# Optimization experiments

Measured on AMD Instinct MI355X. Metric: run time of the kernel, lower is better.

The kernel has to match this reference:

```python
import jax, jax.numpy as jnp
import numpy as np

N_NODES = 50000
N_EDGES = 800000
IN_CH = 128
HID = 32
HEADS = 4
OUT_CH = 10
N_GRAPHS = 64
NEG_SLOPE = 0.2  # PyG GATConv default


def setup_inputs() -> dict:
    key = jax.random.key(0)
    ks = jax.random.split(key, 16)
    d = {}
    d["x"] = jax.random.normal(ks[0], (N_NODES, IN_CH), dtype=jnp.float32)
    d["edge_index"] = jax.random.randint(ks[1], (2, N_EDGES), 0, N_NODES, dtype=jnp.int64)
    d["batch"] = jnp.sort(jax.random.randint(ks[2], (N_NODES,), 0, N_GRAPHS, dtype=jnp.int64))
    s1 = 1.0 / np.sqrt(IN_CH)
    s2 = 1.0 / np.sqrt(HEADS * HID)
    d["W1"] = jax.random.normal(ks[3], (IN_CH, HEADS * HID), dtype=jnp.float32) * s1
    d["att_src1"] = jax.random.normal(ks[4], (HEADS, HID), dtype=jnp.float32) * s2
    d["att_dst1"] = jax.random.normal(ks[5], (HEADS, HID), dtype=jnp.float32) * s2
    d["b1"] = jnp.zeros((HEADS * HID,), dtype=jnp.float32)
    d["W2"] = jax.random.normal(ks[6], (HEADS * HID, HEADS * HID), dtype=jnp.float32) * s2
    d["att_src2"] = jax.random.normal(ks[7], (HEADS, HID), dtype=jnp.float32) * s2
    d["att_dst2"] = jax.random.normal(ks[8], (HEADS, HID), dtype=jnp.float32) * s2
    d["b2"] = jnp.zeros((HEADS * HID,), dtype=jnp.float32)
    d["w_lin"] = jax.random.normal(ks[9], (HEADS * HID, OUT_CH), dtype=jnp.float32) * s2
    d["b_lin"] = jnp.zeros((OUT_CH,), dtype=jnp.float32)
    return d


def _gat_conv(x, src, dst, W, att_src, att_dst, bias):
    # x: [N, Fin] -> h: [N, H, C]
    h = (x @ W).reshape(N_NODES, HEADS, HID)
    a_src = jnp.sum(h * att_src, axis=-1)  # [N, H]
    a_dst = jnp.sum(h * att_dst, axis=-1)  # [N, H]
    e = jax.nn.leaky_relu(a_src[src] + a_dst[dst], NEG_SLOPE)  # [E, H]
    # segment softmax over incoming edges of each destination node
    e_max = jax.ops.segment_max(e, dst, num_segments=N_NODES)  # [N, H]
    e_exp = jnp.exp(e - e_max[dst])
    denom = jax.ops.segment_sum(e_exp, dst, num_segments=N_NODES)  # [N, H]
    alpha = e_exp / denom[dst]  # [E, H]
    # weighted scatter-add aggregation
    out = jax.ops.segment_sum(alpha[:, :, None] * h[src], dst, num_segments=N_NODES)
    return out.reshape(N_NODES, HEADS * HID) + bias


def reference(x, edge_index, batch, W1, att_src1, att_dst1, b1,
              W2, att_src2, att_dst2, b2, w_lin, b_lin):
    # PyG GATConv adds self loops by default
    loops = jnp.arange(N_NODES, dtype=edge_index.dtype)
    src = jnp.concatenate([edge_index[0], loops])
    dst = jnp.concatenate([edge_index[1], loops])

    h = jax.nn.relu(_gat_conv(x, src, dst, W1, att_src1, att_dst1, b1))
    h = jax.nn.relu(_gat_conv(h, src, dst, W2, att_src2, att_dst2, b2))

    # global mean pool over graphs
    sums = jax.ops.segment_sum(h, batch, num_segments=N_GRAPHS)  # [G, H*C]
    counts = jax.ops.segment_sum(jnp.ones((N_NODES,), dtype=h.dtype), batch,
                                 num_segments=N_GRAPHS)
    pooled = sums / jnp.maximum(counts, 1.0)[:, None]

    # dropout is identity in eval mode
    return pooled @ w_lin + b_lin
```

## Files before the change

### kernel.cpp

```cpp
#include <hip/hip_runtime.h>
#include <hip/hip_bf16.h>
#include <math.h>

constexpr int NN = 50000;
constexpr int NE = 800000;
constexpr int ET = NE + NN;
constexpr int FH = 128;
constexpr int NHEAD = 4;
constexpr int NG = 64;
constexpr int OC = 10;

constexpr int NBK = (NN + 255) >> 8;
constexpr int EPB = 4000;
constexpr int HBLK = NE / EPB;

constexpr int WKP = 136;
constexpr int WPLANE = 128 * WKP;

constexpr int GEMM1_GRID = (NN + 255) / 256;
constexpr int GEMM2_GRID = (NN + 63) / 64;

typedef __attribute__((ext_vector_type(8))) short short8;
typedef __attribute__((ext_vector_type(4))) float f32x4;

__device__ inline ushort f2bf_bits(float f) {
    union { __hip_bfloat16 h; ushort u; } c;
    c.h = __float2bfloat16(f);
    return c.u;
}

#define GEMM_EPILOGUE()                                                          \
    float as_[8], ad_[8];                                                        \
    _Pragma("unroll")                                                            \
    for (int t = 0; t < 8; ++t) {                                                \
        as_[t] = att_s[t * 16 + l16];                                            \
        ad_[t] = att_d[t * 16 + l16];                                            \
    }                                                                            \
    float hs[4][4], hd[4][4];                                                    \
    _Pragma("unroll")                                                            \
    for (int r = 0; r < 4; ++r) {                                                \
        int grow = row0 + quad * 4 + r;                                          \
        bool okr = (grow < NN);                                                  \
        _Pragma("unroll")                                                        \
        for (int h = 0; h < 4; ++h) {                                            \
            hs[r][h] = acc[2*h][r] * as_[2*h] + acc[2*h+1][r] * as_[2*h+1];      \
            hd[r][h] = acc[2*h][r] * ad_[2*h] + acc[2*h+1][r] * ad_[2*h+1];      \
        }                                                                        \
        if (okr) {                                                               \
            _Pragma("unroll")                                                    \
            for (int t = 0; t < 8; ++t)                                          \
                Hb[(size_t)grow * FH + t * 16 + l16] = __float2bfloat16(acc[t][r]); \
        }                                                                        \
    }                                                                            \
    _Pragma("unroll")                                                            \
    for (int o = 1; o < 16; o <<= 1) {                                           \
        _Pragma("unroll")                                                        \
        for (int r = 0; r < 4; ++r)                                              \
            _Pragma("unroll")                                                    \
            for (int h = 0; h < 4; ++h) {                                        \
                hs[r][h] += __shfl_xor(hs[r][h], o);                             \
                hd[r][h] += __shfl_xor(hd[r][h], o);                             \
            }                                                                    \
    }                                                                            \
    if (l16 == 0) {                                                              \
        _Pragma("unroll")                                                        \
        for (int r = 0; r < 4; ++r) {                                            \
            int grow = row0 + quad * 4 + r;                                      \
            if (grow < NN) {                                                     \
                *(float4*)&a_src[grow * NHEAD] = make_float4(hs[r][0], hs[r][1], hs[r][2], hs[r][3]); \
                *(float4*)&a_dst[grow * NHEAD] = make_float4(hd[r][0], hd[r][1], hd[r][2], hd[r][3]); \
            }                                                                    \
        }                                                                        \
    }

__global__ __launch_bounds__(1024) void fused_gemm_hist_kernel(
    const int* __restrict__ ei, int* __restrict__ blockHist,
    const float* __restrict__ A, const float* __restrict__ W1,
    const float* __restrict__ W2, ushort* __restrict__ wt,
    const float* __restrict__ att_s, const float* __restrict__ att_d,
    __hip_bfloat16* __restrict__ Hb, float* __restrict__ a_src, float* __restrict__ a_dst)
{
    __shared__ ushort Wlds[2 * WPLANE];
    const int tid = threadIdx.x;

    if (blockIdx.x >= GEMM1_GRID) {
        const int blk = blockIdx.x - GEMM1_GRID;
        int* hist = (int*)Wlds;
        if (tid < NBK) hist[tid] = 0;
        __syncthreads();
        const int e0 = blk * EPB;
        if (tid < EPB / 4) {
            int4 d4 = *(const int4*)(ei + NE + e0 + 4 * tid);
            atomicAdd(&hist[d4.x >> 8], 1);
            atomicAdd(&hist[d4.y >> 8], 1);
            atomicAdd(&hist[d4.z >> 8], 1);
            atomicAdd(&hist[d4.w >> 8], 1);
        }
        if (blk < 64 && tid < 256) {
            int idx = blk * 256 + tid;
            int k = idx >> 7, n = idx & 127;
            float f = W2[idx];
            ushort hb = f2bf_bits(f);
            union { ushort u; __hip_bfloat16 h; } c; c.u = hb;
            float lo = f - __bfloat162float(c.h);
            wt[n * WKP + k] = hb;
            wt[WPLANE + n * WKP + k] = f2bf_bits(lo);
        }
        __syncthreads();
        if (tid < NBK) blockHist[tid * HBLK + blk] = hist[tid];
        return;
    }

    for (int i = tid; i < FH * 128; i += 1024) {
        int k = i >> 7, n = i & 127;
        float f = W1[i];
        ushort hb = f2bf_bits(f);
        union { ushort u; __hip_bfloat16 h; } c; c.u = hb;
        float lo = f - __bfloat162float(c.h);
        Wlds[n * WKP + k] = hb;
        Wlds[WPLANE + n * WKP + k] = f2bf_bits(lo);
    }
    __syncthreads();

    const int wave = tid >> 6;
    const int lane = tid & 63;
    const int quad = lane >> 4;
    const int l16 = lane & 15;
    const int row0 = blockIdx.x * 256 + wave * 16;

    f32x4 acc[8];
#pragma unroll
    for (int t = 0; t < 8; ++t) acc[t] = (f32x4){0.f, 0.f, 0.f, 0.f};

    int arow = row0 + l16; if (arow >= NN) arow = NN - 1;
    const float* ap = A + (size_t)arow * FH + quad * 8;

#pragma unroll
    for (int kc = 0; kc < 4; ++kc) {
        float4 x0 = *(const float4*)(ap + kc * 32);
        float4 x1 = *(const float4*)(ap + kc * 32 + 4);
        float av[8] = {x0.x, x0.y, x0.z, x0.w, x1.x, x1.y, x1.z, x1.w};
        short8 ah, al;
#pragma unroll
        for (int j = 0; j < 8; ++j) {
            ushort hb = f2bf_bits(av[j]);
            union { ushort u; __hip_bfloat16 h; } c; c.u = hb;
            float lo = av[j] - __bfloat162float(c.h);
            ah[j] = (short)hb;
            al[j] = (short)f2bf_bits(lo);
        }
        const int kof = kc * 32 + quad * 8;
#pragma unroll
        for (int t = 0; t < 8; ++t) {
            const ushort* wp = &Wlds[(t * 16 + l16) * WKP + kof];
            short8 wh = *(const short8*)wp;
            short8 wl = *(const short8*)(wp + WPLANE);
            acc[t] = __builtin_amdgcn_mfma_f32_16x16x32_bf16(ah, wh, acc[t], 0, 0, 0);
            acc[t] = __builtin_amdgcn_mfma_f32_16x16x32_bf16(al, wh, acc[t], 0, 0, 0);
            acc[t] = __builtin_amdgcn_mfma_f32_16x16x32_bf16(ah, wl, acc[t], 0, 0, 0);
        }
    }
    GEMM_EPILOGUE()
}

__global__ __launch_bounds__(256) void scanAB_kernel(const int* __restrict__ bh,
                                                     int* __restrict__ bstart,
                                                     int* __restrict__ ebase,
                                                     int* __restrict__ offs) {
    __shared__ int sd[256];
    __shared__ int bprefix;
    const int b = blockIdx.x, t = threadIdx.x;
    int v = 0;
    if (t < NBK) {
        const int* p = bh + t * HBLK;
        for (int i = 0; i < HBLK; ++i) v += p[i];
    }
    sd[t] = v; __syncthreads();
#pragma unroll
    for (int o = 1; o < 256; o <<= 1) {
        int u = (t >= o) ? sd[t - o] : 0;
        __syncthreads();
        sd[t] += u;
        __syncthreads();
    }
    if (t == b) bprefix = sd[t] - v;
    if (b == 0) {
        if (t < NBK) ebase[t] = sd[t] - v;
        if (t == NBK - 1) ebase[NBK] = sd[t];
        if (t == 0) offs[NN] = ET;
    }
    __syncthreads();
    const int base = bprefix;
    __syncthreads();
    int c = (t < HBLK) ? bh[b * HBLK + t] : 0;
    sd[t] = c; __syncthreads();
#pragma unroll
    for (int o = 1; o < 256; o <<= 1) {
        int u = (t >= o) ? sd[t - o] : 0;
        __syncthreads();
        sd[t] += u;
        __syncthreads();
    }
    if (t < HBLK) bstart[b * HBLK + t] = base + sd[t] - c;
}

__global__ __launch_bounds__(1024) void bucket_scatter_kernel(
    const int* __restrict__ ei, const int* __restrict__ bstart,
    int2* __restrict__ ebuf) {
    __shared__ int cur[NBK];
    const int tid = threadIdx.x;
    const int blk = blockIdx.x;
    for (int i = tid; i < NBK; i += 1024) cur[i] = bstart[i * HBLK + blk];
    __syncthreads();
    const int e0 = blk * EPB;
    if (tid < EPB / 4) {
        int4 d4 = *(const int4*)(ei + NE + e0 + 4 * tid);
        int4 s4 = *(const int4*)(ei + e0 + 4 * tid);
        int ds[4] = {d4.x, d4.y, d4.z, d4.w};
        int ss[4] = {s4.x, s4.y, s4.z, s4.w};
#pragma unroll
        for (int j = 0; j < 4; ++j) {
            int pos = atomicAdd(&cur[ds[j] >> 8], 1);
            ebuf[pos] = make_int2(ss[j], ds[j]);
        }
    }
}

__global__ __launch_bounds__(256) void bucket_csr_kernel(
    const int2* __restrict__ ebuf, const int* __restrict__ ebase,
    int* __restrict__ offs, int* __restrict__ csrc) {
    __shared__ int hist[256];
    __shared__ int sd[256];
    __shared__ int cur[256];
    const int b = blockIdx.x, t = threadIdx.x;
    const int lo = b << 8;
    int psz = NN - lo; if (psz > 256) psz = 256;
    const int e0 = ebase[b], e1 = ebase[b + 1];

    hist[t] = 0;
    __syncthreads();
    for (int k = e0 + t; k < e1; k += 256) {
        int2 e = ebuf[k];
        atomicAdd(&hist[e.y - lo], 1);
    }
    __syncthreads();
    const int d = hist[t];
    sd[t] = d; __syncthreads();
#pragma unroll
    for (int o = 1; o < 256; o <<= 1) {
        int u = (t >= o) ? sd[t - o] : 0;
        __syncthreads();
        sd[t] += u;
        __syncthreads();
    }
    const int ex = sd[t] - d;
    if (t < psz) {
        const int node = lo + t;
        const int o = e0 + ex + node;
        offs[node] = o;
        cur[t] = o;
        csrc[o + d] = node;
    }
    __syncthreads();
    for (int k = e0 + t; k < e1; k += 256) {
        int2 e = ebuf[k];
        int pos = atomicAdd(&cur[e.y - lo], 1);
        csrc[pos] = e.x;
    }
}

__global__ __launch_bounds__(256) void gemm_att_bf16_kernel(
    const __hip_bfloat16* __restrict__ A, const ushort* __restrict__ wt,
    const float* __restrict__ att_s, const float* __restrict__ att_d,
    __hip_bfloat16* __restrict__ Hb, float* __restrict__ a_src, float* __restrict__ a_dst)
{
    __shared__ ushort Wlds[2 * WPLANE];
    const int tid = threadIdx.x;
    {
        const uint4* s = (const uint4*)wt;
        uint4* d = (uint4*)Wlds;
        for (int i = tid; i < 2 * WPLANE / 8; i += 256) d[i] = s[i];
    }
    __syncthreads();

    const int wave = tid >> 6;
    const int lane = tid & 63;
    const int quad = lane >> 4;
    const int l16 = lane & 15;
    const int row0 = blockIdx.x * 64 + wave * 16;

    f32x4 acc[8];
#pragma unroll
    for (int t = 0; t < 8; ++t) acc[t] = (f32x4){0.f, 0.f, 0.f, 0.f};

    int arow = row0 + l16; if (arow >= NN) arow = NN - 1;
    const __hip_bfloat16* ap = A + (size_t)arow * FH + quad * 8;

#pragma unroll
    for (int kc = 0; kc < 4; ++kc) {
        short8 ah = *(const short8*)(ap + kc * 32);
        const int kof = kc * 32 + quad * 8;
#pragma unroll
        for (int t = 0; t < 8; ++t) {
            const ushort* wp = &Wlds[(t * 16 + l16) * WKP + kof];
            short8 wh = *(const short8*)wp;
            short8 wl = *(const short8*)(wp + WPLANE);
            acc[t] = __builtin_amdgcn_mfma_f32_16x16x32_bf16(ah, wh, acc[t], 0, 0, 0);
            acc[t] = __builtin_amdgcn_mfma_f32_16x16x32_bf16(ah, wl, acc[t], 0, 0, 0);
        }
    }
    GEMM_EPILOGUE()
}

__global__ __launch_bounds__(256) void gat_agg_kernel(
    const __hip_bfloat16* __restrict__ Hb, const float* __restrict__ asrc,
    const float* __restrict__ adst, const int* __restrict__ offs,
    const int* __restrict__ csrc, const float* __restrict__ bias,
    __hip_bfloat16* __restrict__ out)
{
    const int wid = threadIdx.x >> 6;
    const int lane = threadIdx.x & 63;
    const int n = blockIdx.x * 4 + wid;

    const int beg = offs[n], end = offs[n + 1];
    const int es = lane >> 4;
    const int fs = lane & 15;
    const int hC = fs >> 2;
    const int f8 = fs * 8;
    const float adC = adst[n * NHEAD + hC];

    float dsum = 0.f;
    float acc[8];
#pragma unroll
    for (int i = 0; i < 8; ++i) acc[i] = 0.f;

    const int last = end - 1;
    const int n8 = (end - beg + 7) >> 3;
    for (int p = 0; p < n8; ++p) {
        const int eA = beg + 8 * p + es;
        const int eB = eA + 4;
        const bool vA = eA < end, vB = eB < end;
        const int sA = csrc[vA ? eA : last];
        const int sB = csrc[vB ? eB : last];
        float aA = asrc[sA * NHEAD + hC] + adC;
        float aB = asrc[sB * NHEAD + hC] + adC;
        aA = aA > 0.f ? aA : 0.2f * aA;
        aB = aB > 0.f ? aB : 0.2f * aB;
        const float wA = vA ? __expf(aA) : 0.f;
        const float wB = vB ? __expf(aB) : 0.f;
        dsum += wA + wB;
        union { uint4 u; __hip_bfloat162 b[4]; } cvA, cvB;
        cvA.u = *(const uint4*)&Hb[(size_t)sA * FH + f8];
        cvB.u = *(const uint4*)&Hb[(size_t)sB * FH + f8];
#pragma unroll
        for (int i = 0; i < 4; ++i) {
            float2 hA = __bfloat1622float2(cvA.b[i]);
            float2 hB2 = __bfloat1622float2(cvB.b[i]);
            acc[2 * i]     = fmaf(wA, hA.x, acc[2 * i]);
            acc[2 * i + 1] = fmaf(wA, hA.y, acc[2 * i + 1]);
            acc[2 * i]     = fmaf(wB, hB2.x, acc[2 * i]);
            acc[2 * i + 1] = fmaf(wB, hB2.y, acc[2 * i + 1]);
        }
    }
    dsum += __shfl_xor(dsum, 1);
    dsum += __shfl_xor(dsum, 2);
    dsum += __shfl_xor(dsum, 16);
    dsum += __shfl_xor(dsum, 32);
#pragma unroll
    for (int i = 0; i < 8; ++i) {
        acc[i] += __shfl_xor(acc[i], 16);
        acc[i] += __shfl_xor(acc[i], 32);
    }
    const float inv = 4.0f / dsum;
    if (es == 0) {
        union { ushort u8[8]; uint4 u; } pk;
#pragma unroll
        for (int i = 0; i < 8; ++i) {
            float v = fmaxf(fmaf(acc[i], inv, bias[f8 + i]), 0.f);
            pk.u8[i] = f2bf_bits(v);
        }
        *(uint4*)&out[(size_t)n * FH + f8] = pk.u;
    }
}

__global__ __launch_bounds__(256) void pool_final_kernel(
    const __hip_bfloat16* __restrict__ X, const int* __restrict__ batch,
    const float* __restrict__ wl, const float* __restrict__ bl,
    float* __restrict__ out)
{
    const int g = blockIdx.x;
    const int t = threadIdx.x;
    int a = 0, b = NN;
    while (a < b) { int m = (a + b) >> 1; if (batch[m] < g) a = m + 1; else b = m; }
    const int gs = a;
    b = NN;
    while (a < b) { int m = (a + b) >> 1; if (batch[m] <= g) a = m + 1; else b = m; }
    const int ge = a;

    const int rg = t >> 4;
    const int l16 = t & 15;
    float acc[8];
#pragma unroll
    for (int i = 0; i < 8; ++i) acc[i] = 0.f;
    for (int r = gs + rg; r < ge; r += 16) {
        union { uint4 u; __hip_bfloat162 bb[4]; } cv;
        cv.u = *(const uint4*)&X[(size_t)r * FH + l16 * 8];
#pragma unroll
        for (int i = 0; i < 4; ++i) {
            float2 f = __bfloat1622float2(cv.bb[i]);
            acc[2 * i]     += f.x;
            acc[2 * i + 1] += f.y;
        }
    }
    __shared__ float red[16][128];
    __shared__ float pl[128];
#pragma unroll
    for (int i = 0; i < 8; ++i) red[rg][l16 * 8 + i] = acc[i];
    __syncthreads();
    if (t < 128) {
        float s = 0.f;
#pragma unroll
        for (int j = 0; j < 16; ++j) s += red[j][t];
        pl[t] = s;
    }
    __syncthreads();
    if (t < OC) {
        float invc = 1.0f / fmaxf((float)(ge - gs), 1.0f);
        float a2 = 0.f;
        for (int k = 0; k < FH; ++k)
            a2 = fmaf(pl[k], wl[k * OC + t], a2);
        out[g * OC + t] = a2 * invc + bl[t];
    }
}

extern "C" void kernel_launch(void* const* d_in, const int* in_sizes, int n_in,
                              void* d_out, int out_size, void* d_ws, size_t ws_size,
                              hipStream_t stream) {
    const float* x       = (const float*)d_in[0];
    const int*   ei      = (const int*)d_in[1];
    const int*   batch   = (const int*)d_in[2];
    const float* W1      = (const float*)d_in[3];
    const float* as1     = (const float*)d_in[4];
    const float* ad1     = (const float*)d_in[5];
    const float* b1      = (const float*)d_in[6];
    const float* W2      = (const float*)d_in[7];
    const float* as2     = (const float*)d_in[8];
    const float* ad2     = (const float*)d_in[9];
    const float* b2      = (const float*)d_in[10];
    const float* wlin    = (const float*)d_in[11];
    const float* blin    = (const float*)d_in[12];
    float* out = (float*)d_out;

    __hip_bfloat16* hbuf = (__hip_bfloat16*)d_ws;
    __hip_bfloat16* abuf = hbuf + (size_t)NN * FH;
    float* asrc  = (float*)(abuf + (size_t)NN * FH);
    float* adst  = asrc + (size_t)NN * NHEAD;
    int* offs    = (int*)(adst + (size_t)NN * NHEAD);
    int* csrc    = offs + NN + 1;
    int2* ebuf   = (int2*)(((uintptr_t)(csrc + ET) + 7) & ~(uintptr_t)7);
    int* bh      = (int*)(ebuf + NE);
    int* bstart  = bh + NBK * HBLK;
    int* ebase   = bstart + NBK * HBLK;
    ushort* wt   = (ushort*)(((uintptr_t)(ebase + NBK + 1) + 15) & ~(uintptr_t)15);

    fused_gemm_hist_kernel<<<GEMM1_GRID + HBLK, 1024, 0, stream>>>(
        ei, bh, x, W1, W2, wt, as1, ad1, hbuf, asrc, adst);

    scanAB_kernel<<<NBK, 256, 0, stream>>>(bh, bstart, ebase, offs);
    bucket_scatter_kernel<<<HBLK, 1024, 0, stream>>>(ei, bstart, ebuf);
    bucket_csr_kernel<<<NBK, 256, 0, stream>>>(ebuf, ebase, offs, csrc);

    const int agg_grid = NN / 4;

    gat_agg_kernel<<<agg_grid, 256, 0, stream>>>(hbuf, asrc, adst, offs, csrc, b1, abuf);
    gemm_att_bf16_kernel<<<GEMM2_GRID, 256, 0, stream>>>(abuf, wt, as2, ad2, hbuf, asrc, adst);
    gat_agg_kernel<<<agg_grid, 256, 0, stream>>>(hbuf, asrc, adst, offs, csrc, b2, abuf);

    pool_final_kernel<<<NG, 256, 0, stream>>>(abuf, batch, wlin, blin, out);
}
```

Baseline: 253.2 us.

## Fuse layer-1 GAT aggregation into layer-2 GEMM via LDS tile

New measurement: 271.5 us. +7.2%, slower.

```diff
diff --git a/kernel.cpp b/kernel.cpp
--- a/kernel.cpp
+++ b/kernel.cpp
@@ -17,8 +17,9 @@
 constexpr int WKP = 136;
 constexpr int WPLANE = 128 * WKP;
 
+constexpr int AKP = 136;
+
 constexpr int GEMM1_GRID = (NN + 255) / 256;
-constexpr int GEMM2_GRID = (NN + 63) / 64;
 
 typedef __attribute__((ext_vector_type(8))) short short8;
 typedef __attribute__((ext_vector_type(4))) float f32x4;
@@ -80,7 +81,7 @@
     const float* __restrict__ att_s, const float* __restrict__ att_d,
     __hip_bfloat16* __restrict__ Hb, float* __restrict__ a_src, float* __restrict__ a_dst)
 {
-    __shared__ ushort Wlds[2 * WPLANE];
+    __shared__ __align__(16) ushort Wlds[2 * WPLANE];
     const int tid = threadIdx.x;
 
     if (blockIdx.x >= GEMM1_GRID) {
@@ -269,32 +270,99 @@
     }
 }
 
-__global__ __launch_bounds__(256) void gemm_att_bf16_kernel(
-    const __hip_bfloat16* __restrict__ A, const ushort* __restrict__ wt,
+__global__ __launch_bounds__(1024) void fused_agg_gemm_kernel(
+    const __hip_bfloat16* __restrict__ Hb1, const float* __restrict__ asrc,
+    const float* __restrict__ adst, const int* __restrict__ offs,
+    const int* __restrict__ csrc, const float* __restrict__ bias,
+    const ushort* __restrict__ wt,
     const float* __restrict__ att_s, const float* __restrict__ att_d,
     __hip_bfloat16* __restrict__ Hb, float* __restrict__ a_src, float* __restrict__ a_dst)
 {
-    __shared__ ushort Wlds[2 * WPLANE];
+    __shared__ __align__(16) ushort Wlds[2 * WPLANE];
+    __shared__ __align__(16) ushort Atile[256 * AKP];
     const int tid = threadIdx.x;
     {
         const uint4* s = (const uint4*)wt;
         uint4* d = (uint4*)Wlds;
-        for (int i = tid; i < 2 * WPLANE / 8; i += 256) d[i] = s[i];
-    }
-    __syncthreads();
-
+        for (int i = tid; i < 2 * WPLANE / 8; i += 1024) d[i] = s[i];
+    }
     const int wave = tid >> 6;
     const int lane = tid & 63;
+    const int es = lane >> 4;
+    const int fs = lane & 15;
+    const int hC = fs >> 2;
+    const int f8 = fs * 8;
+
+    for (int j = 0; j < 16; ++j) {
+        const int nl = j * 16 + wave;
+        const int n = blockIdx.x * 256 + nl;
+        if (n < NN) {
+            const int beg = offs[n], end = offs[n + 1];
+            const float adC = adst[n * NHEAD + hC];
+            float dsum = 0.f;
+            float acc[8];
+#pragma unroll
+            for (int i = 0; i < 8; ++i) acc[i] = 0.f;
+            const int last = end - 1;
+            const int n8 = (end - beg + 7) >> 3;
+            for (int p = 0; p < n8; ++p) {
+                const int eA = beg + 8 * p + es;
+                const int eB = eA + 4;
+                const bool vA = eA < end, vB = eB < end;
+                const int sA = csrc[vA ? eA : last];
+                const int sB = csrc[vB ? eB : last];
+                float aA = asrc[sA * NHEAD + hC] + adC;
+                float aB = asrc[sB * NHEAD + hC] + adC;
+                aA = aA > 0.f ? aA : 0.2f * aA;
+                aB = aB > 0.f ? aB : 0.2f * aB;
+                const float wA = vA ? __expf(aA) : 0.f;
+                const float wB = vB ? __expf(aB) : 0.f;
+                dsum += wA + wB;
+                union { uint4 u; __hip_bfloat162 b[4]; } cvA, cvB;
+                cvA.u = *(const uint4*)&Hb1[(size_t)sA * FH + f8];
+                cvB.u = *(const uint4*)&Hb1[(size_t)sB * FH + f8];
+#pragma unroll
+                for (int i = 0; i < 4; ++i) {
+                    float2 hA = __bfloat1622float2(cvA.b[i]);
+                    float2 hB2 = __bfloat1622float2(cvB.b[i]);
+                    acc[2 * i]     = fmaf(wA, hA.x, acc[2 * i]);
+                    acc[2 * i + 1] = fmaf(wA, hA.y, acc[2 * i + 1]);
+                    acc[2 * i]     = fmaf(wB, hB2.x, acc[2 * i]);
+                    acc[2 * i + 1] = fmaf(wB, hB2.y, acc[2 * i + 1]);
+                }
+            }
+            dsum += __shfl_xor(dsum, 1);
+            dsum += __shfl_xor(dsum, 2);
+            dsum += __shfl_xor(dsum, 16);
+            dsum += __shfl_xor(dsum, 32);
+#pragma unroll
+            for (int i = 0; i < 8; ++i) {
+                acc[i] += __shfl_xor(acc[i], 16);
+                acc[i] += __shfl_xor(acc[i], 32);
+            }
+            const float inv = 4.0f / dsum;
+            if (es == 0) {
+                union { ushort u8[8]; uint4 u; } pk;
+#pragma unroll
+                for (int i = 0; i < 8; ++i) {
+                    float v = fmaxf(fmaf(acc[i], inv, bias[f8 + i]), 0.f);
+                    pk.u8[i] = f2bf_bits(v);
+                }
+                *(uint4*)&Atile[nl * AKP + f8] = pk.u;
+            }
+        }
+    }
+    __syncthreads();
+
     const int quad = lane >> 4;
     const int l16 = lane & 15;
-    const int row0 = blockIdx.x * 64 + wave * 16;
+    const int row0 = blockIdx.x * 256 + wave * 16;
 
     f32x4 acc[8];
 #pragma unroll
     for (int t = 0; t < 8; ++t) acc[t] = (f32x4){0.f, 0.f, 0.f, 0.f};
 
-    int arow = row0 + l16; if (arow >= NN) arow = NN - 1;
-    const __hip_bfloat16* ap = A + (size_t)arow * FH + quad * 8;
+    const ushort* ap = &Atile[(wave * 16 + l16) * AKP + quad * 8];
 
 #pragma unroll
     for (int kc = 0; kc < 4; ++kc) {
@@ -451,11 +519,14 @@
     const float* blin    = (const float*)d_in[12];
     float* out = (float*)d_out;
 
-    __hip_bfloat16* hbuf = (__hip_bfloat16*)d_ws;
-    __hip_bfloat16* abuf = hbuf + (size_t)NN * FH;
-    float* asrc  = (float*)(abuf + (size_t)NN * FH);
-    float* adst  = asrc + (size_t)NN * NHEAD;
-    int* offs    = (int*)(adst + (size_t)NN * NHEAD);
+    __hip_bfloat16* hbuf1 = (__hip_bfloat16*)d_ws;
+    __hip_bfloat16* hbuf2 = hbuf1 + (size_t)NN * FH;
+    __hip_bfloat16* abuf  = hbuf2 + (size_t)NN * FH;
+    float* asrc1 = (float*)(abuf + (size_t)NN * FH);
+    float* adst1 = asrc1 + (size_t)NN * NHEAD;
+    float* asrc2 = adst1 + (size_t)NN * NHEAD;
+    float* adst2 = asrc2 + (size_t)NN * NHEAD;
+    int* offs    = (int*)(adst2 + (size_t)NN * NHEAD);
     int* csrc    = offs + NN + 1;
     int2* ebuf   = (int2*)(((uintptr_t)(csrc + ET) + 7) & ~(uintptr_t)7);
     int* bh      = (int*)(ebuf + NE);
@@ -464,17 +535,16 @@
     ushort* wt   = (ushort*)(((uintptr_t)(ebase + NBK + 1) + 15) & ~(uintptr_t)15);
 
     fused_gemm_hist_kernel<<<GEMM1_GRID + HBLK, 1024, 0, stream>>>(
-        ei, bh, x, W1, W2, wt, as1, ad1, hbuf, asrc, adst);
+        ei, bh, x, W1, W2, wt, as1, ad1, hbuf1, asrc1, adst1);
 
     scanAB_kernel<<<NBK, 256, 0, stream>>>(bh, bstart, ebase, offs);
     bucket_scatter_kernel<<<HBLK, 1024, 0, stream>>>(ei, bstart, ebuf);
     bucket_csr_kernel<<<NBK, 256, 0, stream>>>(ebuf, ebase, offs, csrc);
 
-    const int agg_grid = NN / 4;
-
-    gat_agg_kernel<<<agg_grid, 256, 0, stream>>>(hbuf, asrc, adst, offs, csrc, b1, abuf);
-    gemm_att_bf16_kernel<<<GEMM2_GRID, 256, 0, stream>>>(abuf, wt, as2, ad2, hbuf, asrc, adst);
-    gat_agg_kernel<<<agg_grid, 256, 0, stream>>>(hbuf, asrc, adst, offs, csrc, b2, abuf);
+    fused_agg_gemm_kernel<<<GEMM1_GRID, 1024, 0, stream>>>(
+        hbuf1, asrc1, adst1, offs, csrc, b1, wt, as2, ad2, hbuf2, asrc2, adst2);
+
+    gat_agg_kernel<<<NN / 4, 256, 0, stream>>>(hbuf2, asrc2, adst2, offs, csrc, b2, abuf);
 
     pool_final_kernel<<<NG, 256, 0, stream>>>(abuf, batch, wlin, blin, out);
 }
```
